# Optimization experiments

Measured on AMD Instinct MI355X. Metric: run time of the kernel, lower is better.

The kernel has to match this reference:

```python
import jax, jax.numpy as jnp
import numpy as np

E = 1024   # embed_dim
H = 8      # att_heads
HD = E // H
L = 4      # layer_num
B = 64
M = 256
EPS = 1e-5


def celu(x, alpha=1.3):
    return jnp.where(x > 0, x, alpha * jnp.expm1(x / alpha))


def group_norm(x, w, b):
    # x: [N, E], groups = H (GroupNorm over channel groups, per-sample)
    xg = x.reshape(-1, H, HD)
    mu = xg.mean(-1, keepdims=True)
    var = ((xg - mu) ** 2).mean(-1, keepdims=True)
    xg = (xg - mu) * jax.lax.rsqrt(var + EPS)
    return xg.reshape(-1, E) * w + b


def layer_norm(x, w, b):
    mu = x.mean(-1, keepdims=True)
    var = ((x - mu) ** 2).mean(-1, keepdims=True)
    return (x - mu) * jax.lax.rsqrt(var + EPS) * w + b


def setup_inputs() -> dict:
    key = jax.random.key(0)
    ks = jax.random.split(key, 20)
    s = 0.02
    return {
        "gv_feat": jnp.zeros((B, 1), jnp.float32),
        "att_feats": jax.random.normal(ks[0], (B, M, E), jnp.float32),
        "att_mask": jnp.ones((B, M), jnp.float32),
        "mem_W": jax.random.normal(ks[1], (L, E, E), jnp.float32) * s,
        "mem_b": jnp.zeros((L, E), jnp.float32),
        "gn_w": jnp.ones((L, E), jnp.float32),
        "gn_b": jnp.zeros((L, E), jnp.float32),
        "upd_W": jax.random.normal(ks[2], (L, 2 * HD, HD), jnp.float32) * s,
        "upd_b": jnp.zeros((L, HD), jnp.float32),
        "gate_W": jax.random.normal(ks[3], (L, 2 * HD, HD), jnp.float32) * s,
        "gate_b": jnp.zeros((L, HD), jnp.float32),
        "ln_w": jnp.ones((L, E), jnp.float32),
        "ln_b": jnp.zeros((L, E), jnp.float32),
        "proj_W": jax.random.normal(ks[4], ((L + 1) * E, E), jnp.float32) * s,
        "proj_b": jnp.zeros((E,), jnp.float32),
        "lnf_w": jnp.ones((E,), jnp.float32),
        "lnf_b": jnp.zeros((E,), jnp.float32),
    }


def reference(gv_feat, att_feats, att_mask, mem_W, mem_b, gn_w, gn_b,
              upd_W, upd_b, gate_W, gate_b, ln_w, ln_b,
              proj_W, proj_b, lnf_w, lnf_b):
    scaling = HD ** (-0.5)
    mask3 = att_mask[:, :, None]                       # [B, M, 1]
    msum = mask3.sum(1)                                # [B, 1]

    def pool(x):
        return (x * mask3).sum(1) / msum               # [B, E]

    # gv_feat has last dim 1 -> computed by masked mean pooling
    gv = pool(att_feats)
    feat_arr = [gv]
    x = att_feats
    key_mask = att_mask[:, None, None, :]              # [B, 1, 1, M]
    for i in range(L):
        mem = celu(x.reshape(-1, E) @ mem_W[i] + mem_b[i])
        mem = group_norm(mem, gn_w[i], gn_b[i])
        xh = x.reshape(B, M, H, HD).swapaxes(1, 2)     # [B, H, M, HD]
        mh = mem.reshape(B, M, H, HD).swapaxes(1, 2)   # [B, H, M, HD]
        attn = jnp.einsum('bhqd,bhkd->bhqk', xh, mh) * scaling
        attn = jnp.where(key_mask == 0, -1e9, attn)
        p = jax.nn.softmax(attn, axis=-1)
        ctx = jnp.einsum('bhqk,bhkd->bhqd', p, xh)     # values == xh
        inp = jnp.concatenate([xh, ctx], axis=-1)      # [B, H, M, 2*HD]
        f_t = jnp.tanh(jax.nn.relu(inp @ upd_W[i] + upd_b[i]))  # dropout = eval identity
        g_t = jax.nn.sigmoid(inp @ gate_W[i] + gate_b[i])
        xh = g_t * f_t + (1.0 - g_t) * xh
        x = xh.swapaxes(1, 2).reshape(B, M, E)
        x = layer_norm(x, ln_w[i], ln_b[i])
        feat_arr.append(pool(x))
    gv = jnp.concatenate(feat_arr, axis=-1) @ proj_W + proj_b
    gv = layer_norm(gv, lnf_w, lnf_b)
    return gv, x
```

## Files before the change

### kernel.cpp

```cpp
#include <hip/hip_runtime.h>
#include <hip/hip_bf16.h>
#include <cstdint>
#include <cstddef>

typedef __bf16 v8bf __attribute__((ext_vector_type(8)));
typedef __bf16 v4bf __attribute__((ext_vector_type(4)));
typedef float  f32x4 __attribute__((ext_vector_type(4)));

typedef __attribute__((address_space(1))) void gas_void;
typedef __attribute__((address_space(3))) void las_void;

__device__ __forceinline__ void gload_lds16(const void* g, void* l) {
  __builtin_amdgcn_global_load_lds((const gas_void*)g, (las_void*)l, 16, 0, 0);
}

__device__ __forceinline__ float rdv(const void* p, size_t idx, int isf) {
  return isf ? ((const float*)p)[idx] : (float)((const __bf16*)p)[idx];
}

#define PB 64
#define PM 256
#define PE 1024
#define PH 8
#define PHD 128

__global__ void detect_kernel(const void* mask, int* flags) {
  if (threadIdx.x == 0) {
    uint32_t w = *(const uint32_t*)mask;
    flags[0] = ((w >> 16) == 0x3F80u && (w & 0xFFFFu) == 0x3F80u) ? 0 : 1;
  }
}

__global__ __launch_bounds__(256) void convx_kernel(
    const void* __restrict__ src, const int* __restrict__ flags, __bf16* __restrict__ dst) {
  const size_t i = ((size_t)blockIdx.x * 256 + threadIdx.x) * 4;
  if (flags[0]) {
    const float* s = (const float*)src + i;
    v4bf o; o[0] = (__bf16)s[0]; o[1] = (__bf16)s[1]; o[2] = (__bf16)s[2]; o[3] = (__bf16)s[3];
    *(v4bf*)(dst + i) = o;
  } else {
    *(v4bf*)(dst + i) = *(const v4bf*)((const __bf16*)src + i);
  }
}

__global__ __launch_bounds__(256) void transpose_kernel(
    const void* __restrict__ src, size_t soff, size_t zsrc, const int* __restrict__ flags,
    __bf16* __restrict__ dst, size_t zdst, int K, int N) {
  __shared__ __bf16 tile[64][66];
  const int isf = flags[0];
  const size_t so = soff + (size_t)blockIdx.z * zsrc;
  __bf16* d = dst + (size_t)blockIdx.z * zdst;
  const int n0 = blockIdx.x * 64, k0 = blockIdx.y * 64;
  const int c = threadIdx.x & 63, r0 = threadIdx.x >> 6;
#pragma unroll
  for (int j = 0; j < 16; ++j) {
    const int r = j * 4 + r0;
    tile[r][c] = (__bf16)rdv(src, so + (size_t)(k0 + r) * N + (n0 + c), isf);
  }
  __syncthreads();
#pragma unroll
  for (int j = 0; j < 16; ++j) {
    const int r = j * 4 + r0;
    d[(size_t)(n0 + r) * K + k0 + c] = tile[c][r];
  }
}

__global__ __launch_bounds__(256) void ugtr_kernel(
    const void* __restrict__ updW, const void* __restrict__ gateW,
    const int* __restrict__ flags, __bf16* __restrict__ ugWt) {
  __shared__ __bf16 tile[64][66];
  const int isf = flags[0];
  const int z = blockIdx.z, i = z >> 1, g = z & 1;
  const void* src = g ? gateW : updW;
  const size_t soff = (size_t)i * 32768;
  __bf16* dst = ugWt + (size_t)i * 65536 + g * 32768;
  const int n0 = blockIdx.x * 64, k0 = blockIdx.y * 64;
  const int c = threadIdx.x & 63, r0 = threadIdx.x >> 6;
#pragma unroll
  for (int j = 0; j < 16; ++j) {
    const int r = j * 4 + r0;
    tile[r][c] = (__bf16)rdv(src, soff + (size_t)(k0 + r) * 128 + (n0 + c), isf);
  }
  __syncthreads();
#pragma unroll
  for (int j = 0; j < 16; ++j) {
    const int r = j * 4 + r0;
    dst[(size_t)(n0 + r) * 256 + k0 + c] = tile[c][r];
  }
}

template<int AMODE, int BMODE, int ACT, bool OUTF32, bool CLAMPM, bool GNF, bool SPLITK>
__global__ __launch_bounds__(256) void gemm_kernel(
    const __bf16* __restrict__ A, const __bf16* __restrict__ A2,
    const __bf16* __restrict__ Bt,
    const void* __restrict__ bias_a, int offa, const void* __restrict__ bias_b, int offb,
    int bias_split, const int* __restrict__ flags,
    const void* __restrict__ gnw, const void* __restrict__ gnb, int gnoff,
    void* __restrict__ Cout, int K, int Kfull, int Ntot, int Mtot)
{
  __shared__ __align__(16) uint8_t a_s[2][16384];
  __shared__ __align__(16) uint8_t b_s[2][16384];
  __shared__ float gnsum[128][2];
  __shared__ float gnsq[128][2];
  const int mbase = blockIdx.x * 128;
  const int nbase = blockIdx.y * 128;
  const int koff = SPLITK ? blockIdx.z * K : 0;
  const int tid = threadIdx.x;
  const int wid = tid >> 6, lane = tid & 63;
  const int wr = wid >> 1, wc = wid & 1;

  f32x4 acc[4][4];
#pragma unroll
  for (int m = 0; m < 4; ++m)
#pragma unroll
    for (int n = 0; n < 4; ++n) acc[m][n] = (f32x4){0.f, 0.f, 0.f, 0.f};

  const int nkt = K >> 6;
  const int lrow8 = lane >> 3;
  const int cc = (lane & 7) << 4;

  auto STAGE = [&](int kt, uint8_t* as, uint8_t* bs) {
    const int kbase = koff + (kt << 6);
#pragma unroll
    for (int j = 0; j < 4; ++j) {
      const int q = wid * 4 + j;
      const int row = q * 8 + lrow8;
      const int c = cc ^ ((row & 7) << 4);
      const int klocal = c >> 1;
      const __bf16* asrc;
      if (AMODE == 0) {
        int rg = mbase + row;
        if (CLAMPM && rg > Mtot - 1) rg = Mtot - 1;
        asrc = A + (size_t)rg * Kfull + (kbase + klocal);
      } else {
        const int rg = mbase + row;
        const int kg = kbase + klocal;
        if (kg < PHD) {
          const int bh = rg >> 8, mm = rg & 255;
          const int bb = bh >> 3, hh = bh & 7;
          asrc = A + ((size_t)(bb * PM + mm) * PE + hh * PHD + kg);
        } else {
          asrc = A2 + ((size_t)rg * PHD + (kg - PHD));
        }
      }
      gload_lds16(asrc, as + q * 1024);
      const __bf16* bsrc;
      if (BMODE == 0) {
        bsrc = Bt + (size_t)(nbase + row) * Kfull + (kbase + klocal);
      } else {
        bsrc = Bt + (size_t)(mbase >> 8) * (PHD * PM)
                  + (size_t)(nbase + row) * Kfull + (kbase + klocal);
      }
      gload_lds16(bsrc, bs + q * 1024);
    }
  };

  STAGE(0, a_s[0], b_s[0]);
  asm volatile("s_waitcnt vmcnt(0)" ::: "memory");
  __builtin_amdgcn_s_barrier();

  int cur = 0;
  for (int kt = 0; kt < nkt; ++kt) {
    if (kt + 1 < nkt) STAGE(kt + 1, a_s[cur ^ 1], b_s[cur ^ 1]);
    const uint8_t* ap = a_s[cur];
    const uint8_t* bp = b_s[cur];
#pragma unroll
    for (int kk = 0; kk < 2; ++kk) {
      const int co = kk * 64 + ((lane >> 4) << 4);
      v8bf af[4], bfr[4];
#pragma unroll
      for (int m = 0; m < 4; ++m) {
        const int row = wr * 64 + m * 16 + (lane & 15);
        af[m] = *(const v8bf*)(ap + row * 128 + (co ^ ((row & 7) << 4)));
      }
#pragma unroll
      for (int n = 0; n < 4; ++n) {
        const int row = wc * 64 + n * 16 + (lane & 15);
        bfr[n] = *(const v8bf*)(bp + row * 128 + (co ^ ((row & 7) << 4)));
      }
#pragma unroll
      for (int m = 0; m < 4; ++m)
#pragma unroll
        for (int n = 0; n < 4; ++n)
          acc[m][n] = __builtin_amdgcn_mfma_f32_16x16x32_bf16(af[m], bfr[n], acc[m][n], 0, 0, 0);
    }
    asm volatile("s_waitcnt vmcnt(0)" ::: "memory");
    __builtin_amdgcn_s_barrier();
    cur ^= 1;
  }

  const int isf = flags[0];
  if constexpr (GNF) {
    float bv[4];
#pragma unroll
    for (int n = 0; n < 4; ++n) {
      const int col = nbase + wc * 64 + n * 16 + (lane & 15);
      bv[n] = (bias_a != nullptr) ? rdv(bias_a, offa + col, isf) : 0.f;
    }
#pragma unroll
    for (int m = 0; m < 4; ++m)
#pragma unroll
      for (int n = 0; n < 4; ++n)
#pragma unroll
        for (int r = 0; r < 4; ++r) {
          float v = acc[m][n][r] + bv[n];
          if (ACT == 1) v = (v > 0.f) ? v : 1.3f * expm1f(v * (1.0f / 1.3f));
          acc[m][n][r] = v;
        }
#pragma unroll
    for (int m = 0; m < 4; ++m)
#pragma unroll
      for (int r = 0; r < 4; ++r) {
        float s = 0.f, q = 0.f;
#pragma unroll
        for (int n = 0; n < 4; ++n) { s += acc[m][n][r]; q += acc[m][n][r] * acc[m][n][r]; }
#pragma unroll
        for (int off = 1; off < 16; off <<= 1) {
          s += __shfl_xor(s, off, 64); q += __shfl_xor(q, off, 64);
        }
        const int lrow = wr * 64 + m * 16 + ((lane >> 4) << 2) + r;
        if ((lane & 15) == 0) { gnsum[lrow][wc] = s; gnsq[lrow][wc] = q; }
      }
    __syncthreads();
#pragma unroll
    for (int m = 0; m < 4; ++m)
#pragma unroll
      for (int r = 0; r < 4; ++r) {
        const int lrow = wr * 64 + m * 16 + ((lane >> 4) << 2) + r;
        const float mean = (gnsum[lrow][0] + gnsum[lrow][1]) * (1.f / 128.f);
        const float var = (gnsq[lrow][0] + gnsq[lrow][1]) * (1.f / 128.f) - mean * mean;
        const float rstd = rsqrtf(var + 1e-5f);
        const int rg = mbase + lrow;
#pragma unroll
        for (int n = 0; n < 4; ++n) {
          const int col = nbase + wc * 64 + n * 16 + (lane & 15);
          const float o = (acc[m][n][r] - mean) * rstd * rdv(gnw, gnoff + col, isf)
                          + rdv(gnb, gnoff + col, isf);
          ((__bf16*)Cout)[(size_t)rg * Ntot + col] = (__bf16)o;
        }
      }
  } else {
    float* coutF = (float*)Cout + (SPLITK ? (size_t)blockIdx.z * 65536 : (size_t)0);
#pragma unroll
    for (int m = 0; m < 4; ++m) {
      const int rowt = mbase + wr * 64 + m * 16 + ((lane >> 4) << 2);
#pragma unroll
      for (int n = 0; n < 4; ++n) {
        const int col = nbase + wc * 64 + n * 16 + (lane & 15);
        float bvv = 0.f;
        if (bias_a != nullptr)
          bvv = (col < bias_split) ? rdv(bias_a, offa + col, isf)
                                   : rdv(bias_b, offb + col - bias_split, isf);
#pragma unroll
        for (int r = 0; r < 4; ++r) {
          const int rg = rowt + r;
          if (CLAMPM && rg >= Mtot) continue;
          float v = acc[m][n][r] + bvv;
          if (ACT == 1) v = (v > 0.f) ? v : 1.3f * expm1f(v * (1.0f / 1.3f));
          if (OUTF32) coutF[(size_t)rg * Ntot + col] = v;
          else        ((__bf16*)Cout)[(size_t)rg * Ntot + col] = (__bf16)v;
        }
      }
    }
  }
}

__global__ __launch_bounds__(256) void attn_softmax_kernel(
    const __bf16* __restrict__ xc, const __bf16* __restrict__ memc,
    const void* __restrict__ mask, const int* __restrict__ flags, int b0,
    __bf16* __restrict__ S)
{
  const int bhl = blockIdx.x;
  const int bl = bhl >> 3, h = bhl & 7;
  const int isf = flags[0];
  const int tid = threadIdx.x, wid = tid >> 6, lane = tid & 63;
  const int qbase = blockIdx.y * 64 + wid * 16;
  const size_t xoff = (size_t)bl * PM * PE + h * PHD;

  v8bf a[4];
  {
    const int row = qbase + (lane & 15);
    const int d0 = (lane >> 4) * 8;
    const __bf16* p = xc + xoff + (size_t)row * PE + d0;
#pragma unroll
    for (int k = 0; k < 4; ++k) a[k] = *(const v8bf*)(p + k * 32);
  }
  float mz[16];
#pragma unroll
  for (int t = 0; t < 16; ++t)
    mz[t] = rdv(mask, (size_t)(b0 + bl) * PM + t * 16 + (lane & 15), isf);

  f32x4 acc[16];
#pragma unroll
  for (int t = 0; t < 16; ++t) acc[t] = (f32x4){0.f, 0.f, 0.f, 0.f};
#pragma unroll
  for (int t = 0; t < 16; ++t) {
    const int key = t * 16 + (lane & 15);
    const int d0 = (lane >> 4) * 8;
    const __bf16* p = memc + xoff + (size_t)key * PE + d0;
#pragma unroll
    for (int k = 0; k < 4; ++k) {
      v8bf bb = *(const v8bf*)(p + k * 32);
      acc[t] = __builtin_amdgcn_mfma_f32_16x16x32_bf16(a[k], bb, acc[t], 0, 0, 0);
    }
  }
  const float scale = 0.08838834764831845f;
  float mx[4], sm[4];
#pragma unroll
  for (int r = 0; r < 4; ++r) mx[r] = -3.0e38f;
#pragma unroll
  for (int t = 0; t < 16; ++t)
#pragma unroll
    for (int r = 0; r < 4; ++r) {
      float v = (mz[t] == 0.f) ? -1.0e9f : acc[t][r] * scale;
      acc[t][r] = v;
      mx[r] = fmaxf(mx[r], v);
    }
#pragma unroll
  for (int off = 1; off < 16; off <<= 1)
#pragma unroll
    for (int r = 0; r < 4; ++r) mx[r] = fmaxf(mx[r], __shfl_xor(mx[r], off, 64));
#pragma unroll
  for (int r = 0; r < 4; ++r) sm[r] = 0.f;
#pragma unroll
  for (int t = 0; t < 16; ++t)
#pragma unroll
    for (int r = 0; r < 4; ++r) {
      float e = expf(acc[t][r] - mx[r]);
      acc[t][r] = e; sm[r] += e;
    }
#pragma unroll
  for (int off = 1; off < 16; off <<= 1)
#pragma unroll
    for (int r = 0; r < 4; ++r) sm[r] += __shfl_xor(sm[r], off, 64);
#pragma unroll
  for (int r = 0; r < 4; ++r) sm[r] = 1.f / sm[r];

  const size_t srow = (size_t)bhl * PM;
#pragma unroll
  for (int r = 0; r < 4; ++r) {
    const int q = qbase + (lane >> 4) * 4 + r;
    __bf16* sp = S + (srow + q) * PM;
#pragma unroll
    for (int t = 0; t < 16; ++t)
      sp[t * 16 + (lane & 15)] = (__bf16)(acc[t][r] * sm[r]);
  }
}

__global__ __launch_bounds__(256) void transpose_x_kernel(
    const __bf16* __restrict__ xc, __bf16* __restrict__ xT)
{
  const int bh = blockIdx.x;
  const int b = bh >> 3, h = bh & 7;
  const int tz = blockIdx.y;
  const int d0 = (tz & 1) * 64, m0 = (tz >> 1) * 64;
  __shared__ __bf16 tile[64][66];
  const int c = threadIdx.x & 63, r0 = threadIdx.x >> 6;
  const __bf16* src = xc + ((size_t)b * PM + m0) * PE + h * PHD + d0;
#pragma unroll
  for (int j = 0; j < 16; ++j) {
    const int r = j * 4 + r0;
    tile[r][c] = src[(size_t)r * PE + c];
  }
  __syncthreads();
  __bf16* dst = xT + ((size_t)bh * PHD + d0) * PM + m0;
#pragma unroll
  for (int j = 0; j < 16; ++j) {
    const int r = j * 4 + r0;
    dst[(size_t)r * PM + c] = tile[c][r];
  }
}

__global__ __launch_bounds__(256) void gatingln_kernel(
    const __bf16* __restrict__ ug, const __bf16* __restrict__ xc,
    const void* __restrict__ w, const void* __restrict__ bz, int off,
    const int* __restrict__ flags, __bf16* __restrict__ xout,
    void* __restrict__ outAux, int row0)
{
  const size_t row = blockIdx.x;
  const int tid = threadIdx.x, wid = tid >> 6, lane = tid & 63;
  const int isf = flags[0];
  const int e = tid * 4, h = tid >> 5, d = e & 127;
  const size_t b = row >> 8; const int m = (int)(row & 255);
  const size_t ugrow = ((b * PH + h) * PM + m);
  v4bf fv = *(const v4bf*)(ug + ugrow * 256 + d);
  v4bf gvv = *(const v4bf*)(ug + ugrow * 256 + 128 + d);
  v4bf xv = *(const v4bf*)(xc + row * PE + e);
  float o[4];
#pragma unroll
  for (int r = 0; r < 4; ++r) {
    float f = fv[r], g = gvv[r], xh = xv[r];
    float gs = 1.f / (1.f + expf(-g));
    float ft = tanhf(fmaxf(f, 0.f));
    o[r] = gs * ft + (1.f - gs) * xh;
  }
  float s = o[0] + o[1] + o[2] + o[3];
  float q = o[0] * o[0] + o[1] * o[1] + o[2] * o[2] + o[3] * o[3];
#pragma unroll
  for (int off2 = 1; off2 < 64; off2 <<= 1) {
    s += __shfl_xor(s, off2, 64); q += __shfl_xor(q, off2, 64);
  }
  __shared__ float ss[4], qq[4];
  if (lane == 0) { ss[wid] = s; qq[wid] = q; }
  __syncthreads();
  s = ss[0] + ss[1] + ss[2] + ss[3];
  q = qq[0] + qq[1] + qq[2] + qq[3];
  const float mean = s * (1.f / 1024.f);
  const float var = q * (1.f / 1024.f) - mean * mean;
  const float rstd = rsqrtf(var + 1e-5f);
  float ov[4];
#pragma unroll
  for (int r = 0; r < 4; ++r)
    ov[r] = (o[r] - mean) * rstd * rdv(w, off + e + r, isf) + rdv(bz, off + e + r, isf);
  v4bf vo; vo[0] = (__bf16)ov[0]; vo[1] = (__bf16)ov[1]; vo[2] = (__bf16)ov[2]; vo[3] = (__bf16)ov[3];
  *(v4bf*)(xout + row * PE + e) = vo;
  if (outAux != nullptr) {
    const size_t idx = 65536 + (size_t)(row0 + row) * PE + e;
    if (isf) {
      float* op = (float*)outAux;
      op[idx] = ov[0]; op[idx + 1] = ov[1]; op[idx + 2] = ov[2]; op[idx + 3] = ov[3];
    } else {
      __bf16* op = (__bf16*)outAux;
      op[idx] = (__bf16)ov[0]; op[idx + 1] = (__bf16)ov[1];
      op[idx + 2] = (__bf16)ov[2]; op[idx + 3] = (__bf16)ov[3];
    }
  }
}

__global__ void msum_kernel(const void* __restrict__ mask, const int* __restrict__ flags,
                            float* __restrict__ msum)
{
  const int b = blockIdx.x, t = threadIdx.x;
  const int isf = flags[0];
  float s = 0.f;
#pragma unroll
  for (int j = 0; j < 4; ++j) s += rdv(mask, (size_t)b * PM + j * 64 + t, isf);
#pragma unroll
  for (int off = 1; off < 64; off <<= 1) s += __shfl_xor(s, off, 64);
  if (t == 0) msum[b] = s;
}

__global__ __launch_bounds__(1024) void pool_kernel(
    const __bf16* __restrict__ x, const void* __restrict__ mask, const int* __restrict__ flags,
    const float* __restrict__ msum, __bf16* __restrict__ feats, int colOff)
{
  __shared__ float red[4][256];
  const int b = blockIdx.x;
  const int el = threadIdx.x & 255;
  const int wq = threadIdx.x >> 8;
  const int e = blockIdx.y * 256 + el;
  const int isf = flags[0];
  const __bf16* p = x + (size_t)b * PM * PE + e;
  float acc = 0.f;
  const int m0 = wq * 64;
  for (int m = m0; m < m0 + 64; m += 4) {
#pragma unroll
    for (int j = 0; j < 4; ++j)
      acc += (float)p[(size_t)(m + j) * PE] * rdv(mask, (size_t)b * PM + m + j, isf);
  }
  red[wq][el] = acc;
  __syncthreads();
  if (wq == 0) {
    float s = red[0][el] + red[1][el] + red[2][el] + red[3][el];
    feats[(size_t)b * (5 * PE) + colOff + e] = (__bf16)(s / msum[b]);
  }
}

__global__ __launch_bounds__(256) void projreduce_kernel(
    const float* __restrict__ part, const void* __restrict__ pb,
    const int* __restrict__ flags, float* __restrict__ gvpre)
{
  const int row = blockIdx.x;
  const int c0 = threadIdx.x * 4;
  const int isf = flags[0];
  float a0 = rdv(pb, c0 + 0, isf), a1 = rdv(pb, c0 + 1, isf);
  float a2 = rdv(pb, c0 + 2, isf), a3 = rdv(pb, c0 + 3, isf);
#pragma unroll
  for (int z = 0; z < 8; ++z) {
    const float* p = part + (size_t)z * 65536 + (size_t)row * 1024 + c0;
    a0 += p[0]; a1 += p[1]; a2 += p[2]; a3 += p[3];
  }
  float* op = gvpre + (size_t)row * 1024 + c0;
  op[0] = a0; op[1] = a1; op[2] = a2; op[3] = a3;
}

__global__ __launch_bounds__(256) void ln_final_kernel(
    const float* __restrict__ gin, const void* __restrict__ w, const void* __restrict__ bz,
    const int* __restrict__ flags, void* __restrict__ out)
{
  const size_t row = blockIdx.x;
  const int tid = threadIdx.x, wid = tid >> 6, lane = tid & 63;
  const int isf = flags[0];
  const float* p = gin + row * PE + tid * 4;
  float f0 = p[0], f1 = p[1], f2 = p[2], f3 = p[3];
  float s = f0 + f1 + f2 + f3;
  float q = f0 * f0 + f1 * f1 + f2 * f2 + f3 * f3;
#pragma unroll
  for (int off = 1; off < 64; off <<= 1) {
    s += __shfl_xor(s, off, 64); q += __shfl_xor(q, off, 64);
  }
  __shared__ float ss[4], qq[4];
  if (lane == 0) { ss[wid] = s; qq[wid] = q; }
  __syncthreads();
  s = ss[0] + ss[1] + ss[2] + ss[3];
  q = qq[0] + qq[1] + qq[2] + qq[3];
  const float mean = s * (1.f / 1024.f);
  const float var = q * (1.f / 1024.f) - mean * mean;
  const float rstd = rsqrtf(var + 1e-5f);
  const int e = tid * 4;
#pragma unroll
  for (int j = 0; j < 4; ++j) {
    const float fj = (j == 0 ? f0 : j == 1 ? f1 : j == 2 ? f2 : f3);
    const float ov = (fj - mean) * rstd * rdv(w, e + j, isf) + rdv(bz, e + j, isf);
    if (isf) ((float*)out)[row * PE + e + j] = ov;
    else     ((__bf16*)out)[row * PE + e + j] = (__bf16)ov;
  }
}

extern "C" void kernel_launch(void* const* d_in, const int* in_sizes, int n_in,
                              void* d_out, int out_size, void* d_ws, size_t ws_size,
                              hipStream_t stream) {
  const void* att_feats = d_in[1];
  const void* att_mask  = d_in[2];
  const void* mem_W  = d_in[3];
  const void* mem_b  = d_in[4];
  const void* gn_w   = d_in[5];
  const void* gn_b   = d_in[6];
  const void* upd_W  = d_in[7];
  const void* upd_b  = d_in[8];
  const void* gate_W = d_in[9];
  const void* gate_b = d_in[10];
  const void* ln_w   = d_in[11];
  const void* ln_b   = d_in[12];
  const void* proj_W = d_in[13];
  const void* proj_b = d_in[14];
  const void* lnf_w  = d_in[15];
  const void* lnf_b  = d_in[16];

  uint8_t* ws = (uint8_t*)d_ws;
  int*    flags  = (int*)ws;
  float*  msum   = (float*)(ws + 4096);
  __bf16* featsb = (__bf16*)(ws + 8192);
  float*  gvpre  = (float*)(ws + 665600);
  __bf16* memWt  = (__bf16*)(ws + 1048576);
  __bf16* ugWt   = (__bf16*)(ws + 9437184);
  __bf16* xa0    = (__bf16*)(ws + 10485760);
  __bf16* xa     = (__bf16*)(ws + 44040192);
  uint8_t* dynb  = ws + 77594624;

  int NC;
  if (ws_size >= (size_t)211812352) NC = 1;
  else if (ws_size >= (size_t)144703488) NC = 2;
  else NC = 4;
  const int CSd = PB / NC;
  const int CROWSd = CSd * PM;
  const int CGRd = CSd * PH * PM;
  const size_t CB = (size_t)CROWSd * PE * 2;
  __bf16* membc = (__bf16*)dynb;
  __bf16* xTgc  = (__bf16*)(dynb + CB);
  __bf16* sbufc = (__bf16*)(dynb + 2 * CB);

  detect_kernel<<<1, 64, 0, stream>>>(att_mask, flags);
  convx_kernel<<<16384, 256, 0, stream>>>(att_feats, flags, xa0);

  transpose_kernel<<<dim3(16, 16, 4), 256, 0, stream>>>(
      mem_W, 0, 1048576, flags, memWt, 1048576, 1024, 1024);
  ugtr_kernel<<<dim3(2, 4, 8), 256, 0, stream>>>(upd_W, gate_W, flags, ugWt);

  msum_kernel<<<64, 64, 0, stream>>>(att_mask, flags, msum);
  pool_kernel<<<dim3(64, 4), 1024, 0, stream>>>(xa0, att_mask, flags, msum, featsb, 0);

  const __bf16* xcur = xa0;
  for (int i = 0; i < 4; ++i) {
    for (int c = 0; c < NC; ++c) {
      const __bf16* xc = xcur + (size_t)c * CROWSd * PE;
      gemm_kernel<0, 0, 1, false, false, true, false><<<dim3(CROWSd / 128, 8), 256, 0, stream>>>(
          xc, nullptr, memWt + (size_t)i * 1048576, mem_b, i * 1024, nullptr, 0, 1024,
          flags, gn_w, gn_b, i * 1024, membc, 1024, 1024, 1024, CROWSd);
      transpose_x_kernel<<<dim3(CSd * 8, 8), 256, 0, stream>>>(xc, xTgc);
      attn_softmax_kernel<<<dim3(CSd * 8, 4), 256, 0, stream>>>(xc, membc, att_mask, flags,
                                                                c * CSd, sbufc);
      gemm_kernel<0, 1, 0, false, false, false, false><<<dim3(CGRd / 128, 1), 256, 0, stream>>>(
          sbufc, nullptr, xTgc, nullptr, 0, nullptr, 0, 128, flags, nullptr, nullptr, 0,
          membc, 256, 256, 128, CGRd);
      gemm_kernel<1, 0, 0, false, false, false, false><<<dim3(CGRd / 128, 2), 256, 0, stream>>>(
          xc, membc, ugWt + (size_t)i * 65536, upd_b, i * 128, gate_b, i * 128, 128,
          flags, nullptr, nullptr, 0, sbufc, 256, 256, 256, CGRd);
      gatingln_kernel<<<CROWSd, 256, 0, stream>>>(sbufc, xc, ln_w, ln_b, i * 1024, flags,
                                                  xa + (size_t)c * CROWSd * PE,
                                                  (i == 3) ? d_out : nullptr, c * CROWSd);
    }
    pool_kernel<<<dim3(64, 4), 1024, 0, stream>>>(xa, att_mask, flags, msum, featsb,
                                                  (i + 1) * 1024);
    xcur = xa;
  }

  __bf16* projWt = sbufc;
  float* projPart = (float*)dynb;
  transpose_kernel<<<dim3(16, 80, 1), 256, 0, stream>>>(proj_W, 0, 0, flags, projWt, 0, 5120, 1024);
  gemm_kernel<0, 0, 0, true, true, false, true><<<dim3(1, 8, 8), 256, 0, stream>>>(
      featsb, nullptr, projWt, nullptr, 0, nullptr, 0, 1024,
      flags, nullptr, nullptr, 0, projPart, 640, 5120, 1024, 64);
  projreduce_kernel<<<64, 256, 0, stream>>>(projPart, proj_b, flags, gvpre);
  ln_final_kernel<<<64, 256, 0, stream>>>(gvpre, lnf_w, lnf_b, flags, d_out);
}
```

Measured before the change: 1.379 ms.

## Deepen GEMM prefetch to two stages and swizzle block order per XCD

```diff
diff --git a/kernel.cpp b/kernel.cpp
--- a/kernel.cpp
+++ b/kernel.cpp
@@ -89,7 +89,7 @@
   }
 }
 
-template<int AMODE, int BMODE, int ACT, bool OUTF32, bool CLAMPM, bool GNF, bool SPLITK>
+template<int AMODE, int BMODE, int ACT, bool OUTF32, bool CLAMPM, bool GNF, bool SPLITK, bool SWZ>
 __global__ __launch_bounds__(256) void gemm_kernel(
     const __bf16* __restrict__ A, const __bf16* __restrict__ A2,
     const __bf16* __restrict__ Bt,
@@ -102,8 +102,16 @@
   __shared__ __align__(16) uint8_t b_s[2][16384];
   __shared__ float gnsum[128][2];
   __shared__ float gnsq[128][2];
-  const int mbase = blockIdx.x * 128;
-  const int nbase = blockIdx.y * 128;
+  int bx = blockIdx.x, by = blockIdx.y;
+  if (SWZ) {
+    const int nx = gridDim.x;
+    const int flat = by * nx + bx;
+    const int xcd = flat & 7, slot = flat >> 3;
+    by = slot & 7;
+    bx = (slot >> 3) * 8 + xcd;
+  }
+  const int mbase = bx * 128;
+  const int nbase = by * 128;
   const int koff = SPLITK ? blockIdx.z * K : 0;
   const int tid = threadIdx.x;
   const int wid = tid >> 6, lane = tid & 63;
@@ -156,14 +164,15 @@
   };
 
   STAGE(0, a_s[0], b_s[0]);
-  asm volatile("s_waitcnt vmcnt(0)" ::: "memory");
-  __builtin_amdgcn_s_barrier();
-
-  int cur = 0;
+  if (nkt > 1) STAGE(1, a_s[1], b_s[1]);
+
   for (int kt = 0; kt < nkt; ++kt) {
-    if (kt + 1 < nkt) STAGE(kt + 1, a_s[cur ^ 1], b_s[cur ^ 1]);
-    const uint8_t* ap = a_s[cur];
-    const uint8_t* bp = b_s[cur];
+    if (kt + 1 < nkt) asm volatile("s_waitcnt vmcnt(8)" ::: "memory");
+    else              asm volatile("s_waitcnt vmcnt(0)" ::: "memory");
+    __builtin_amdgcn_s_barrier();
+    __builtin_amdgcn_sched_barrier(0);
+    const uint8_t* ap = a_s[kt & 1];
+    const uint8_t* bp = b_s[kt & 1];
 #pragma unroll
     for (int kk = 0; kk < 2; ++kk) {
       const int co = kk * 64 + ((lane >> 4) << 4);
@@ -184,9 +193,9 @@
         for (int n = 0; n < 4; ++n)
           acc[m][n] = __builtin_amdgcn_mfma_f32_16x16x32_bf16(af[m], bfr[n], acc[m][n], 0, 0, 0);
     }
-    asm volatile("s_waitcnt vmcnt(0)" ::: "memory");
     __builtin_amdgcn_s_barrier();
-    cur ^= 1;
+    __builtin_amdgcn_sched_barrier(0);
+    if (kt + 2 < nkt) STAGE(kt + 2, a_s[kt & 1], b_s[kt & 1]);
   }
 
   const int isf = flags[0];
@@ -574,16 +583,16 @@
   for (int i = 0; i < 4; ++i) {
     for (int c = 0; c < NC; ++c) {
       const __bf16* xc = xcur + (size_t)c * CROWSd * PE;
-      gemm_kernel<0, 0, 1, false, false, true, false><<<dim3(CROWSd / 128, 8), 256, 0, stream>>>(
+      gemm_kernel<0, 0, 1, false, false, true, false, true><<<dim3(CROWSd / 128, 8), 256, 0, stream>>>(
           xc, nullptr, memWt + (size_t)i * 1048576, mem_b, i * 1024, nullptr, 0, 1024,
           flags, gn_w, gn_b, i * 1024, membc, 1024, 1024, 1024, CROWSd);
       transpose_x_kernel<<<dim3(CSd * 8, 8), 256, 0, stream>>>(xc, xTgc);
       attn_softmax_kernel<<<dim3(CSd * 8, 4), 256, 0, stream>>>(xc, membc, att_mask, flags,
                                                                 c * CSd, sbufc);
-      gemm_kernel<0, 1, 0, false, false, false, false><<<dim3(CGRd / 128, 1), 256, 0, stream>>>(
+      gemm_kernel<0, 1, 0, false, false, false, false, false><<<dim3(CGRd / 128, 1), 256, 0, stream>>>(
           sbufc, nullptr, xTgc, nullptr, 0, nullptr, 0, 128, flags, nullptr, nullptr, 0,
           membc, 256, 256, 128, CGRd);
-      gemm_kernel<1, 0, 0, false, false, false, false><<<dim3(CGRd / 128, 2), 256, 0, stream>>>(
+      gemm_kernel<1, 0, 0, false, false, false, false, false><<<dim3(CGRd / 128, 2), 256, 0, stream>>>(
           xc, membc, ugWt + (size_t)i * 65536, upd_b, i * 128, gate_b, i * 128, 128,
           flags, nullptr, nullptr, 0, sbufc, 256, 256, 256, CGRd);
       gatingln_kernel<<<CROWSd, 256, 0, stream>>>(sbufc, xc, ln_w, ln_b, i * 1024, flags,
@@ -598,7 +607,7 @@
   __bf16* projWt = sbufc;
   float* projPart = (float*)dynb;
   transpose_kernel<<<dim3(16, 80, 1), 256, 0, stream>>>(proj_W, 0, 0, flags, projWt, 0, 5120, 1024);
-  gemm_kernel<0, 0, 0, true, true, false, true><<<dim3(1, 8, 8), 256, 0, stream>>>(
+  gemm_kernel<0, 0, 0, true, true, false, true, false><<<dim3(1, 8, 8), 256, 0, stream>>>(
       featsb, nullptr, projWt, nullptr, 0, nullptr, 0, 1024,
       flags, nullptr, nullptr, 0, projPart, 640, 5120, 1024, 64);
   projreduce_kernel<<<64, 256, 0, stream>>>(projPart, proj_b, flags, gvpre);
```

Measured after the change: 1.427 ms. +3.5%, slower.
